# Kernel tuning notes

Hardware: AMD Instinct MI355X
Metric: run time of the kernel (lower is better)

Reference implementation:

```python
import jax, jax.numpy as jnp
import numpy as np

N = 8192


def setup_inputs() -> dict:
    key = jax.random.key(0)
    k1, k2 = jax.random.split(key)
    # dense symmetric-style weight matrix (adjacency/Laplacian analog)
    info_mtx = jax.random.uniform(k1, (N, N), dtype=jnp.float32)
    state = jax.random.normal(k2, (N,), dtype=jnp.float32)
    return {"info_mtx": info_mtx, "state": state}


def reference(info_mtx, state):
    # pb_type == 'maxcut': G = -0.5 * info_mtx
    G = -0.5 * info_mtx
    # Original python loop: sum over i<=j of G[i,j]*s_i*s_j (diag term linear in s_i)
    offdiag = jnp.triu(G, k=1)                     # strictly upper triangle [N,N]
    diag = jnp.diagonal(G)                         # [N]
    quad = jnp.dot(state, offdiag @ state)         # sum_{i<j} G_ij s_i s_j
    lin = jnp.dot(diag, state)                     # sum_i G_ii s_i
    total = -(quad + lin)
    num_edges = jnp.sum(info_mtx) / 2.0
    return num_edges / 2.0 - total
```

## Files before the change

### kernel.cpp

```cpp
#include <hip/hip_runtime.h>


static constexpr int N_DIM = 8192;
static constexpr int VPR   = N_DIM / 4;
static constexpr int BLOCK = 256;
static constexpr int ITERS = VPR / BLOCK;
static constexpr int FBLOCK = 1024;

__global__ __launch_bounds__(BLOCK) void ising_row_kernel(
    const float4* __restrict__ mtx4,
    const float*  __restrict__ state,
    float*        __restrict__ partial)
{
    const int   row = blockIdx.x;
    const int   d   = row >> 2;
    const float p   = -0.5f * state[row];
    const float4* __restrict__ rowp = mtx4 + (size_t)row * VPR;
    const float4* __restrict__ s4   = (const float4*)state;

    float4 m[ITERS];
    float4 s[ITERS];
#pragma unroll
    for (int k = 0; k < ITERS; ++k)
        m[k] = rowp[threadIdx.x + (k << 8)];
#pragma unroll
    for (int k = 0; k < ITERS; ++k)
        s[k] = s4[threadIdx.x + (k << 8)];

    float accA  = 0.0f;
    float accQ0 = 0.0f, accQ1 = 0.0f;
#pragma unroll
    for (int k = 0; k < ITERS; ++k) {
        const int    v  = threadIdx.x + (k << 8);
        const float4 mm = m[k];
        const float4 sj = s[k];
        accA += (mm.x + mm.y) + (mm.z + mm.w);
        if (v > d) {
            accQ0 = fmaf(mm.x, sj.x, accQ0);
            accQ1 = fmaf(mm.y, sj.y, accQ1);
            accQ0 = fmaf(mm.z, sj.z, accQ0);
            accQ1 = fmaf(mm.w, sj.w, accQ1);
        } else if (v == d) {
            const int j0 = v << 2;
            float w;
            w = (j0 + 0 > row) ? sj.x : ((j0 + 0 == row) ? 1.0f : 0.0f);
            accQ0 = fmaf(mm.x, w, accQ0);
            w = (j0 + 1 > row) ? sj.y : ((j0 + 1 == row) ? 1.0f : 0.0f);
            accQ1 = fmaf(mm.y, w, accQ1);
            w = (j0 + 2 > row) ? sj.z : ((j0 + 2 == row) ? 1.0f : 0.0f);
            accQ0 = fmaf(mm.z, w, accQ0);
            w = (j0 + 3 > row) ? sj.w : ((j0 + 3 == row) ? 1.0f : 0.0f);
            accQ1 = fmaf(mm.w, w, accQ1);
        }
    }

    float acc = fmaf(0.25f, accA, p * (accQ0 + accQ1));

    for (int off = 32; off > 0; off >>= 1)
        acc += __shfl_down(acc, off, 64);

    __shared__ float lds[BLOCK / 64];
    const int lane = threadIdx.x & 63;
    const int wave = threadIdx.x >> 6;
    if (lane == 0) lds[wave] = acc;
    __syncthreads();
    if (threadIdx.x == 0)
        partial[blockIdx.x] = (lds[0] + lds[1]) + (lds[2] + lds[3]);
}

__global__ __launch_bounds__(FBLOCK) void ising_final_kernel(
    const float* __restrict__ partial,
    float*       __restrict__ out)
{
    float acc = 0.0f;
#pragma unroll
    for (int k = 0; k < N_DIM / FBLOCK; ++k)
        acc += partial[threadIdx.x + k * FBLOCK];

    for (int off = 32; off > 0; off >>= 1)
        acc += __shfl_down(acc, off, 64);

    __shared__ float lds[FBLOCK / 64];
    const int lane = threadIdx.x & 63;
    const int wave = threadIdx.x >> 6;
    if (lane == 0) lds[wave] = acc;
    __syncthreads();
    if (threadIdx.x == 0) {
        float sum = 0.0f;
#pragma unroll
        for (int w = 0; w < FBLOCK / 64; ++w) sum += lds[w];
        out[0] = sum;
    }
}

extern "C" void kernel_launch(void* const* d_in, const int* in_sizes, int n_in,
                              void* d_out, int out_size, void* d_ws, size_t ws_size,
                              hipStream_t stream) {
    const float* mtx   = (const float*)d_in[0];
    const float* state = (const float*)d_in[1];
    float* out     = (float*)d_out;
    float* partial = (float*)d_ws;

    ising_row_kernel<<<N_DIM, BLOCK, 0, stream>>>((const float4*)mtx, state, partial);
    ising_final_kernel<<<1, FBLOCK, 0, stream>>>(partial, out);
}
```

Measured before the change: 349.8 us.

## Process multiple rows per block with double-buffered register prefetch

Switches from one block per row to 1024 blocks that each handle 8 rows. The state vector is loaded once per block, and the next row is prefetched into a second register buffer while the current one is reduced. The final kernel now reads only 1024 partials. This aims to cut redundant state loads and per-block launch and reduction overhead, and to keep memory loads in flight across rows. The cost is higher register pressure from the two 8-float4 buffers plus the state buffer, which may reduce occupancy.

```diff
diff --git a/kernel.cpp b/kernel.cpp
--- a/kernel.cpp
+++ b/kernel.cpp
@@ -1,70 +1,103 @@
 #include <hip/hip_runtime.h>
 
 
-static constexpr int N_DIM = 8192;
-static constexpr int VPR   = N_DIM / 4;
-static constexpr int BLOCK = 256;
-static constexpr int ITERS = VPR / BLOCK;
+static constexpr int N_DIM  = 8192;
+static constexpr int VPR    = N_DIM / 4;
+static constexpr int BLOCK  = 256;
+static constexpr int ITERS  = VPR / BLOCK;
+static constexpr int GRID   = 1024;
+static constexpr int RPB    = N_DIM / GRID;
 static constexpr int FBLOCK = 1024;
 
-__global__ __launch_bounds__(BLOCK) void ising_row_kernel(
+__device__ __forceinline__ float row_term(
+    const float4 (&m)[ITERS], const float4 (&s)[ITERS],
+    const int tid, const int row, const float p)
+{
+    const int d = row >> 2;
+    float accA = 0.0f, q0 = 0.0f, q1 = 0.0f;
+#pragma unroll
+    for (int k = 0; k < ITERS; ++k) {
+        const int    v  = tid + (k << 8);
+        const float4 mm = m[k];
+        const float4 sj = s[k];
+        accA += (mm.x + mm.y) + (mm.z + mm.w);
+        if (v > d) {
+            q0 = fmaf(mm.x, sj.x, q0);
+            q1 = fmaf(mm.y, sj.y, q1);
+            q0 = fmaf(mm.z, sj.z, q0);
+            q1 = fmaf(mm.w, sj.w, q1);
+        } else if (v == d) {
+            const int j0 = v << 2;
+            float w;
+            w = (j0 + 0 > row) ? sj.x : ((j0 + 0 == row) ? 1.0f : 0.0f);
+            q0 = fmaf(mm.x, w, q0);
+            w = (j0 + 1 > row) ? sj.y : ((j0 + 1 == row) ? 1.0f : 0.0f);
+            q1 = fmaf(mm.y, w, q1);
+            w = (j0 + 2 > row) ? sj.z : ((j0 + 2 == row) ? 1.0f : 0.0f);
+            q0 = fmaf(mm.z, w, q0);
+            w = (j0 + 3 > row) ? sj.w : ((j0 + 3 == row) ? 1.0f : 0.0f);
+            q1 = fmaf(mm.w, w, q1);
+        }
+    }
+    return fmaf(0.25f, accA, p * (q0 + q1));
+}
+
+__global__ __launch_bounds__(BLOCK, 4) void ising_rows_kernel(
     const float4* __restrict__ mtx4,
     const float*  __restrict__ state,
     float*        __restrict__ partial)
 {
-    const int   row = blockIdx.x;
-    const int   d   = row >> 2;
-    const float p   = -0.5f * state[row];
-    const float4* __restrict__ rowp = mtx4 + (size_t)row * VPR;
-    const float4* __restrict__ s4   = (const float4*)state;
+    const int tid = threadIdx.x;
+    const float4* __restrict__ s4 = (const float4*)state;
 
-    float4 m[ITERS];
     float4 s[ITERS];
 #pragma unroll
     for (int k = 0; k < ITERS; ++k)
-        m[k] = rowp[threadIdx.x + (k << 8)];
+        s[k] = s4[tid + (k << 8)];
+
+    const int row0 = blockIdx.x * RPB;
+    const float4* __restrict__ base = mtx4 + (size_t)row0 * VPR;
+
+    float4 mA[ITERS], mB[ITERS];
 #pragma unroll
     for (int k = 0; k < ITERS; ++k)
-        s[k] = s4[threadIdx.x + (k << 8)];
+        mA[k] = base[tid + (k << 8)];
 
-    float accA  = 0.0f;
-    float accQ0 = 0.0f, accQ1 = 0.0f;
+    float acc = 0.0f;
+
+    for (int g = 0; g < RPB; g += 2) {
 #pragma unroll
-    for (int k = 0; k < ITERS; ++k) {
-        const int    v  = threadIdx.x + (k << 8);
-        const float4 mm = m[k];
-        const float4 sj = s[k];
-        accA += (mm.x + mm.y) + (mm.z + mm.w);
-        if (v > d) {
-            accQ0 = fmaf(mm.x, sj.x, accQ0);
-            accQ1 = fmaf(mm.y, sj.y, accQ1);
-            accQ0 = fmaf(mm.z, sj.z, accQ0);
-            accQ1 = fmaf(mm.w, sj.w, accQ1);
-        } else if (v == d) {
-            const int j0 = v << 2;
-            float w;
-            w = (j0 + 0 > row) ? sj.x : ((j0 + 0 == row) ? 1.0f : 0.0f);
-            accQ0 = fmaf(mm.x, w, accQ0);
-            w = (j0 + 1 > row) ? sj.y : ((j0 + 1 == row) ? 1.0f : 0.0f);
-            accQ1 = fmaf(mm.y, w, accQ1);
-            w = (j0 + 2 > row) ? sj.z : ((j0 + 2 == row) ? 1.0f : 0.0f);
-            accQ0 = fmaf(mm.z, w, accQ0);
-            w = (j0 + 3 > row) ? sj.w : ((j0 + 3 == row) ? 1.0f : 0.0f);
-            accQ1 = fmaf(mm.w, w, accQ1);
+        for (int k = 0; k < ITERS; ++k)
+            mB[k] = base[(g + 1) * VPR + tid + (k << 8)];
+
+        {
+            const int   row = row0 + g;
+            const float p   = -0.5f * state[row];
+            acc += row_term(mA, s, tid, row, p);
+        }
+
+        if (g + 2 < RPB) {
+#pragma unroll
+            for (int k = 0; k < ITERS; ++k)
+                mA[k] = base[(g + 2) * VPR + tid + (k << 8)];
+        }
+
+        {
+            const int   row = row0 + g + 1;
+            const float p   = -0.5f * state[row];
+            acc += row_term(mB, s, tid, row, p);
         }
     }
-
-    float acc = fmaf(0.25f, accA, p * (accQ0 + accQ1));
 
     for (int off = 32; off > 0; off >>= 1)
         acc += __shfl_down(acc, off, 64);
 
     __shared__ float lds[BLOCK / 64];
-    const int lane = threadIdx.x & 63;
-    const int wave = threadIdx.x >> 6;
+    const int lane = tid & 63;
+    const int wave = tid >> 6;
     if (lane == 0) lds[wave] = acc;
     __syncthreads();
-    if (threadIdx.x == 0)
+    if (tid == 0)
         partial[blockIdx.x] = (lds[0] + lds[1]) + (lds[2] + lds[3]);
 }
 
@@ -72,10 +105,7 @@
     const float* __restrict__ partial,
     float*       __restrict__ out)
 {
-    float acc = 0.0f;
-#pragma unroll
-    for (int k = 0; k < N_DIM / FBLOCK; ++k)
-        acc += partial[threadIdx.x + k * FBLOCK];
+    float acc = partial[threadIdx.x];
 
     for (int off = 32; off > 0; off >>= 1)
         acc += __shfl_down(acc, off, 64);
@@ -101,6 +131,6 @@
     float* out     = (float*)d_out;
     float* partial = (float*)d_ws;
 
-    ising_row_kernel<<<N_DIM, BLOCK, 0, stream>>>((const float4*)mtx, state, partial);
+    ising_rows_kernel<<<GRID, BLOCK, 0, stream>>>((const float4*)mtx, state, partial);
     ising_final_kernel<<<1, FBLOCK, 0, stream>>>(partial, out);
 }
```

New measurement: 432.6 us. 1.24x slower.
